# Kernel tuning notes

Measured on AMD Instinct MI355X. Metric: run time of the kernel, lower is better.

Reference implementation:

```python
import jax, jax.numpy as jnp
import numpy as np

N = 50000
E = 800000
IN_C, HID, HEADS, CLS = 128, 64, 5, 40
NEG_SLOPE = 0.2


def gat_conv(h, src, dst, W, a_src, a_dst, bias, heads, out_c, concat):
    n = h.shape[0]
    hp = (h @ W).reshape(n, heads, out_c)            # [N,H,C]
    a_s = jnp.sum(hp * a_src, axis=-1)               # [N,H]
    a_d = jnp.sum(hp * a_dst, axis=-1)               # [N,H]
    e = jax.nn.leaky_relu(a_s[src] + a_d[dst], NEG_SLOPE)  # [Etot,H]
    m = jax.ops.segment_max(e, dst, num_segments=n)  # segment softmax over dst
    e = jnp.exp(e - m[dst])
    s = jax.ops.segment_sum(e, dst, num_segments=n)
    alpha = e / (s[dst] + 1e-16)                     # [Etot,H]
    msg = hp[src] * alpha[:, :, None]                # [Etot,H,C]
    out = jax.ops.segment_sum(msg, dst, num_segments=n)
    if concat:
        out = out.reshape(n, heads * out_c)
    else:
        out = out.mean(axis=1)
    return out + bias


def setup_inputs() -> dict:
    key = jax.random.key(0)
    ks = jax.random.split(key, 12)
    x = jax.random.normal(ks[0], (N, IN_C), dtype=jnp.float32)
    edge_index = jax.random.randint(ks[1], (2, E), 0, N, dtype=jnp.int64)
    g = 0.1
    return {
        "x": x,
        "edge_index": edge_index,
        "emb_W": jax.random.normal(ks[2], (IN_C, HID), jnp.float32) * g,
        "emb_b": jnp.zeros((HID,), jnp.float32),
        "W1": jax.random.normal(ks[3], (HID, HEADS * HID), jnp.float32) * g,
        "att_src1": jax.random.normal(ks[4], (HEADS, HID), jnp.float32) * g,
        "att_dst1": jax.random.normal(ks[5], (HEADS, HID), jnp.float32) * g,
        "b1": jnp.zeros((HEADS * HID,), jnp.float32),
        "W2": jax.random.normal(ks[6], (HEADS * HID, HEADS * CLS), jnp.float32) * g,
        "att_src2": jax.random.normal(ks[7], (HEADS, CLS), jnp.float32) * g,
        "att_dst2": jax.random.normal(ks[8], (HEADS, CLS), jnp.float32) * g,
        "b2": jnp.zeros((CLS,), jnp.float32),
    }


def reference(x, edge_index, emb_W, emb_b, W1, att_src1, att_dst1, b1,
              W2, att_src2, att_dst2, b2):
    n = x.shape[0]
    loops = jnp.arange(n, dtype=edge_index.dtype)
    src = jnp.concatenate([edge_index[0], loops])  # PyG adds self-loops
    dst = jnp.concatenate([edge_index[1], loops])
    h = x @ emb_W + emb_b
    emb = h
    # dropout skipped (eval mode)
    h = jax.nn.elu(gat_conv(h, src, dst, W1, att_src1, att_dst1, b1, HEADS, HID, True))
    h = gat_conv(h, src, dst, W2, att_src2, att_dst2, b2, HEADS, CLS, False)
    return emb, jax.nn.log_softmax(h, axis=1)
```

## Files before the change

kernel.cpp:

```cpp
#include <hip/hip_runtime.h>
#include <math.h>

constexpr int N_NODES = 50000;
constexpr int E_EDGES = 800000;
constexpr int ETOT    = E_EDGES + N_NODES;
constexpr int IN_C    = 128;
constexpr int HID     = 64;
constexpr int HEADS   = 5;
constexpr int CLS     = 40;
constexpr int SLOTW   = 96;
constexpr float NEG_SLOPE = 0.2f;

typedef __attribute__((ext_vector_type(8))) short short8;
typedef __attribute__((ext_vector_type(4))) float float4v;
typedef __attribute__((ext_vector_type(2))) float f32x2;

__device__ __forceinline__ float lrelu(float v) {
    return v > 0.f ? v : NEG_SLOPE * v;
}
__device__ __forceinline__ float bf2f(unsigned short u) {
    return __uint_as_float(((unsigned)u) << 16);
}
__device__ __forceinline__ f32x2 bfp2f(unsigned u) {
    f32x2 r;
    r.x = __uint_as_float(u << 16);
    r.y = __uint_as_float(u & 0xFFFF0000u);
    return r;
}
__device__ __forceinline__ unsigned short f2bf(float f) {
    unsigned u = __float_as_uint(f);
    return (unsigned short)((u + 0x7fffu + ((u >> 16) & 1u)) >> 16);
}

__device__ __forceinline__ void pack_one(const float* __restrict__ B,
                                         unsigned short* __restrict__ Bp,
                                         int N, int KS, int t)
{
    int lane = t & 63;
    int f = (t >> 6) & 3;
    int rest = t >> 8;
    int ks = rest % KS;
    int nt = rest / KS;
    int n = nt * 64 + f * 16 + (lane & 15);
    int kbase = ks * 32 + (lane >> 4) * 8;
    unsigned short vals[8];
    #pragma unroll
    for (int j = 0; j < 8; j++) {
        float v = (n < N) ? B[(long)(kbase + j) * N + n] : 0.f;
        vals[j] = f2bf(v);
    }
    *(ushort4*)(Bp + (long)t * 8)     = make_ushort4(vals[0], vals[1], vals[2], vals[3]);
    *(ushort4*)(Bp + (long)t * 8 + 4) = make_ushort4(vals[4], vals[5], vals[6], vals[7]);
}

__global__ void pack_weights(const float* __restrict__ W0, const float* __restrict__ W1,
                             const float* __restrict__ W2,
                             const float* __restrict__ att1s, const float* __restrict__ att1d,
                             const float* __restrict__ att2s, const float* __restrict__ att2d,
                             unsigned short* __restrict__ Bp0,
                             unsigned short* __restrict__ Bp1,
                             unsigned short* __restrict__ Bp2,
                             float* __restrict__ u1s, float* __restrict__ u1d,
                             unsigned short* __restrict__ Bs)
{
    int t = blockIdx.x * blockDim.x + threadIdx.x;
    if (t < 13824) {
        if (t < 1024)      pack_one(W0, Bp0, 64,  4,  t);
        else if (t < 3584) pack_one(W1, Bp1, 320, 2,  t - 1024);
        else               pack_one(W2, Bp2, 200, 10, t - 3584);
    } else if (t < 14464) {
        int i = t - 13824;
        bool isd = i >= 320;
        int j = isd ? i - 320 : i;
        int h = j >> 6, k = j & 63;
        const float* att = isd ? att1d : att1s;
        float sum = 0.f;
        for (int c = 0; c < 64; c++)
            sum += W1[k * 320 + h * 64 + c] * att[h * 64 + c];
        (isd ? u1d : u1s)[j] = sum;
    } else if (t < 15104) {
        int i = t - 14464;
        int lane = i & 63, ks = i >> 6;
        int n = lane & 15, kq = lane >> 4;
        unsigned short vals[8];
        #pragma unroll
        for (int j = 0; j < 8; j++) {
            int k = ks * 32 + kq * 8 + j;
            float sum = 0.f;
            if (n < 5) {
                for (int c = 0; c < 40; c++)
                    sum += W2[k * 200 + n * 40 + c] * att2s[n * 40 + c];
            } else if (n >= 8 && n < 13) {
                int h = n - 8;
                for (int c = 0; c < 40; c++)
                    sum += W2[k * 200 + h * 40 + c] * att2d[h * 40 + c];
            }
            vals[j] = f2bf(sum);
        }
        *(ushort4*)(Bs + (long)i * 8)     = make_ushort4(vals[0], vals[1], vals[2], vals[3]);
        *(ushort4*)(Bs + (long)i * 8 + 4) = make_ushort4(vals[4], vals[5], vals[6], vals[7]);
    }
}

__global__ __launch_bounds__(256) void emb_scatter_fused(
    const float* __restrict__ A, const unsigned short* __restrict__ Bp,
    const float* __restrict__ bias,
    const float* __restrict__ u1s, const float* __restrict__ u1d,
    float* __restrict__ Cf, unsigned short* __restrict__ Cb,
    float* __restrict__ asd, int M,
    const int* __restrict__ ei, int* __restrict__ cnt,
    unsigned short* __restrict__ slots, int nScat)
{
    if ((int)blockIdx.x < nScat) {
        int t = blockIdx.x * 256 + threadIdx.x;
        if (t >= ETOT) return;
        int s, d;
        if (t < E_EDGES) { s = ei[t]; d = ei[E_EDGES + t]; }
        else             { s = d = t - E_EDGES; }
        int pos = atomicAdd(&cnt[d], 1);
        if (pos < SLOTW) slots[d * SLOTW + pos] = (unsigned short)s;
        return;
    }
    const int gb = blockIdx.x - nScat;
    const int K = 128, KS = 4;
    const int w = threadIdx.x >> 6, lane = threadIdx.x & 63;
    const int cl = lane & 15, kq = lane >> 4;
    int rowA = gb * 64 + w * 16 + cl;
    if (rowA >= M) rowA = M - 1;
    const float* ap = A + (long)rowA * K + kq * 8;
    const unsigned short* bp = Bp + lane * 8;
    float4v acc[4] = {};
    #pragma unroll
    for (int ks = 0; ks < KS; ks++) {
        float4 u0 = *(const float4*)(ap + ks * 32);
        float4 u1 = *(const float4*)(ap + ks * 32 + 4);
        short8 a;
        a[0] = f2bf(u0.x); a[1] = f2bf(u0.y); a[2] = f2bf(u0.z); a[3] = f2bf(u0.w);
        a[4] = f2bf(u1.x); a[5] = f2bf(u1.y); a[6] = f2bf(u1.z); a[7] = f2bf(u1.w);
        #pragma unroll
        for (int f = 0; f < 4; f++) {
            short8 b = *(const short8*)(bp + ks * 2048 + f * 512);
            acc[f] = __builtin_amdgcn_mfma_f32_16x16x32_bf16(a, b, acc[f], 0, 0, 0);
        }
    }
    int rbase = gb * 64 + w * 16 + kq * 4;
    float bc4[4];
    #pragma unroll
    for (int f = 0; f < 4; f++) {
        int col = f * 16 + cl;
        float bc = bias[col];
        bc4[f] = bc;
        #pragma unroll
        for (int r = 0; r < 4; r++) {
            int row = rbase + r;
            if (row < M) {
                float v = acc[f][r] + bc;
                Cf[(long)row * 64 + col] = v;
                Cb[(long)row * 64 + col] = f2bf(v);
            }
        }
    }
    #pragma unroll
    for (int h = 0; h < HEADS; h++) {
        float us[4], ud[4];
        #pragma unroll
        for (int f = 0; f < 4; f++) {
            us[f] = u1s[h * 64 + f * 16 + cl];
            ud[f] = u1d[h * 64 + f * 16 + cl];
        }
        #pragma unroll
        for (int r = 0; r < 4; r++) {
            float ps = 0.f, pd = 0.f;
            #pragma unroll
            for (int f = 0; f < 4; f++) {
                float v = acc[f][r] + bc4[f];
                ps += v * us[f];
                pd += v * ud[f];
            }
            #pragma unroll
            for (int off = 1; off < 16; off <<= 1) {
                ps += __shfl_xor(ps, off);
                pd += __shfl_xor(pd, off);
            }
            int row = rbase + r;
            if (cl == 0 && row < M) {
                asd[row * 16 + h]     = ps;
                asd[row * 16 + 8 + h] = pd;
            }
        }
    }
}

__global__ __launch_bounds__(256) void aggr1_new(
    const int* __restrict__ cnt, const unsigned short* __restrict__ slots,
    const float* __restrict__ asd,
    const unsigned short* __restrict__ emb, unsigned short* __restrict__ e_out)
{
    __shared__ float alph[4][64 * 8];
    int wid = (blockIdx.x * blockDim.x + threadIdx.x) >> 6;
    int w = threadIdx.x >> 6;
    int lane = threadIdx.x & 63;
    if (wid >= N_NODES) return;
    int deg = cnt[wid];
    if (deg > SLOTW) deg = SLOTW;
    const unsigned short* myslot = slots + wid * SLOTW;

    float adh[HEADS];
    #pragma unroll
    for (int h = 0; h < HEADS; h++) adh[h] = asd[wid * 16 + 8 + h];

    const char* embB = (const char*)emb;

    if (deg <= 64) {
        bool has = lane < deg;
        int s = has ? (int)myslot[lane] : 0;
        int rowoff = s * 128;
        float4 s4 = *(const float4*)(asd + s * 16);
        float  s5 = asd[s * 16 + 4];
        float v[HEADS], mx[HEADS], sm[HEADS];
        v[0] = has ? lrelu(s4.x + adh[0]) : -1e30f;
        v[1] = has ? lrelu(s4.y + adh[1]) : -1e30f;
        v[2] = has ? lrelu(s4.z + adh[2]) : -1e30f;
        v[3] = has ? lrelu(s4.w + adh[3]) : -1e30f;
        v[4] = has ? lrelu(s5   + adh[4]) : -1e30f;
        #pragma unroll
        for (int h = 0; h < HEADS; h++) mx[h] = v[h];
        if (deg <= 32) {
            #pragma unroll
            for (int h = 0; h < HEADS; h++)
                #pragma unroll
                for (int off = 16; off; off >>= 1)
                    mx[h] = fmaxf(mx[h], __shfl_xor(mx[h], off));
        } else {
            #pragma unroll
            for (int h = 0; h < HEADS; h++)
                #pragma unroll
                for (int off = 32; off; off >>= 1)
                    mx[h] = fmaxf(mx[h], __shfl_xor(mx[h], off));
        }
        #pragma unroll
        for (int h = 0; h < HEADS; h++) {
            float e = has ? __expf(v[h] - mx[h]) : 0.f;
            v[h] = e;
            sm[h] = e;
        }
        if (deg <= 32) {
            #pragma unroll
            for (int h = 0; h < HEADS; h++)
                #pragma unroll
                for (int off = 16; off; off >>= 1)
                    sm[h] += __shfl_xor(sm[h], off);
        } else {
            #pragma unroll
            for (int h = 0; h < HEADS; h++)
                #pragma unroll
                for (int off = 32; off; off >>= 1)
                    sm[h] += __shfl_xor(sm[h], off);
        }
        #pragma unroll
        for (int h = 0; h < HEADS; h++)
            alph[w][lane * 8 + h] = v[h] / (sm[h] + 1e-16f);

        const int g = lane >> 4, cl16 = lane & 15;
        f32x2 av[HEADS][2] = {};
        int nE8 = (deg + 7) & ~7;
        for (int i = 0; i < nE8; i += 8) {
            int e0 = i + g, e1 = i + 4 + g;
            int off0 = __shfl(rowoff, e0);
            int off1 = __shfl(rowoff, e1);
            uint2 q0 = *(const uint2*)(embB + off0 + cl16 * 8);
            uint2 q1 = *(const uint2*)(embB + off1 + cl16 * 8);
            float4 b0 = *(const float4*)&alph[w][e0 * 8];
            float  b4 = alph[w][e0 * 8 + 4];
            float4 c0 = *(const float4*)&alph[w][e1 * 8];
            float  c4 = alph[w][e1 * 8 + 4];
            f32x2 f0a = bfp2f(q0.x), f0b = bfp2f(q0.y);
            f32x2 f1a = bfp2f(q1.x), f1b = bfp2f(q1.y);
            av[0][0] += f0a * b0.x; av[0][1] += f0b * b0.x;
            av[1][0] += f0a * b0.y; av[1][1] += f0b * b0.y;
            av[2][0] += f0a * b0.z; av[2][1] += f0b * b0.z;
            av[3][0] += f0a * b0.w; av[3][1] += f0b * b0.w;
            av[4][0] += f0a * b4;   av[4][1] += f0b * b4;
            av[0][0] += f1a * c0.x; av[0][1] += f1b * c0.x;
            av[1][0] += f1a * c0.y; av[1][1] += f1b * c0.y;
            av[2][0] += f1a * c0.z; av[2][1] += f1b * c0.z;
            av[3][0] += f1a * c0.w; av[3][1] += f1b * c0.w;
            av[4][0] += f1a * c4;   av[4][1] += f1b * c4;
        }
        #pragma unroll
        for (int h = 0; h < HEADS; h++)
            #pragma unroll
            for (int p = 0; p < 2; p++) {
                float tx = av[h][p].x, ty = av[h][p].y;
                tx += __shfl_xor(tx, 16); tx += __shfl_xor(tx, 32);
                ty += __shfl_xor(ty, 16); ty += __shfl_xor(ty, 32);
                av[h][p].x = tx; av[h][p].y = ty;
            }
        if (g == 0) {
            #pragma unroll
            for (int h = 0; h < HEADS; h++) {
                ushort4 o = make_ushort4(f2bf(av[h][0].x), f2bf(av[h][0].y),
                                         f2bf(av[h][1].x), f2bf(av[h][1].y));
                *(ushort4*)(e_out + (long)wid * 320 + h * 64 + cl16 * 4) = o;
            }
        }
    } else {
        float acc[HEADS] = {};
        float mx[HEADS], inv[HEADS], sm[HEADS] = {};
        #pragma unroll
        for (int h = 0; h < HEADS; h++) mx[h] = -1e30f;
        for (int e = lane; e < deg; e += 64) {
            int s = myslot[e];
            #pragma unroll
            for (int h = 0; h < HEADS; h++)
                mx[h] = fmaxf(mx[h], lrelu(asd[s * 16 + h] + adh[h]));
        }
        #pragma unroll
        for (int h = 0; h < HEADS; h++)
            #pragma unroll
            for (int off = 32; off; off >>= 1)
                mx[h] = fmaxf(mx[h], __shfl_xor(mx[h], off));
        for (int e = lane; e < deg; e += 64) {
            int s = myslot[e];
            #pragma unroll
            for (int h = 0; h < HEADS; h++)
                sm[h] += __expf(lrelu(asd[s * 16 + h] + adh[h]) - mx[h]);
        }
        #pragma unroll
        for (int h = 0; h < HEADS; h++) {
            #pragma unroll
            for (int off = 32; off; off >>= 1)
                sm[h] += __shfl_xor(sm[h], off);
            inv[h] = 1.f / (sm[h] + 1e-16f);
        }
        for (int e = 0; e < deg; e++) {
            int s0 = myslot[e];
            float fv = bf2f(*(const unsigned short*)(embB + s0 * 128 + lane * 2));
            #pragma unroll
            for (int h = 0; h < HEADS; h++) {
                float a0 = __expf(lrelu(asd[s0 * 16 + h] + adh[h]) - mx[h]) * inv[h];
                acc[h] += fv * a0;
            }
        }
        #pragma unroll
        for (int h = 0; h < HEADS; h++)
            e_out[(long)wid * 320 + h * 64 + lane] = f2bf(acc[h]);
    }
}

__global__ __launch_bounds__(256, 5) void gemm_mix_l2(
    const unsigned short* __restrict__ A, const unsigned short* __restrict__ Bp1,
    const unsigned short* __restrict__ Bp2, const float* __restrict__ bias,
    const unsigned short* __restrict__ Bs,
    unsigned short* __restrict__ hp2, float* __restrict__ asd, int M)
{
    constexpr int LDP = 328;
    __shared__ unsigned short tile[32 * LDP];
    const int wid = threadIdx.x >> 6, lane = threadIdx.x & 63;
    const int band = wid >> 1, half = wid & 1;
    const int cl = lane & 15, kq = lane >> 4;
    int rowA = blockIdx.x * 32 + band * 16 + cl;
    if (rowA >= M) rowA = M - 1;
    const unsigned short* ap = A + (long)rowA * 320;
    const unsigned short* bp1 = Bp1 + lane * 8;

    const int rbase = blockIdx.x * 32 + band * 16 + kq * 4;
    const int lrow = band * 16 + kq * 4;

    if (half == 0) {
        float4v acc[12] = {};
        #pragma unroll
        for (int i = 0; i < 3; i++)
            #pragma unroll
            for (int ks = 0; ks < 2; ks++) {
                short8 a = *(const short8*)(ap + i * 64 + ks * 32 + kq * 8);
                #pragma unroll
                for (int f = 0; f < 4; f++) {
                    short8 b = *(const short8*)(bp1 + (i * 2 + ks) * 2048 + f * 512);
                    acc[i * 4 + f] =
                        __builtin_amdgcn_mfma_f32_16x16x32_bf16(a, b, acc[i * 4 + f], 0, 0, 0);
                }
            }
        #pragma unroll
        for (int i = 0; i < 3; i++)
            #pragma unroll
            for (int f = 0; f < 4; f++) {
                int col = i * 64 + f * 16 + cl;
                float bc = bias[col];
                #pragma unroll
                for (int r = 0; r < 4; r++) {
                    float v = acc[i * 4 + f][r] + bc;
                    v = v > 0.f ? v : __expf(v) - 1.f;
                    tile[(lrow + r) * LDP + col] = f2bf(v);
                }
            }
    } else {
        float4v acc[8] = {};
        #pragma unroll
        for (int i = 0; i < 2; i++)
            #pragma unroll
            for (int ks = 0; ks < 2; ks++) {
                short8 a = *(const short8*)(ap + (3 + i) * 64 + ks * 32 + kq * 8);
                #pragma unroll
                for (int f = 0; f < 4; f++) {
                    short8 b = *(const short8*)(bp1 + ((3 + i) * 2 + ks) * 2048 + f * 512);
                    acc[i * 4 + f] =
                        __builtin_amdgcn_mfma_f32_16x16x32_bf16(a, b, acc[i * 4 + f], 0, 0, 0);
                }
            }
        #pragma unroll
        for (int i = 0; i < 2; i++)
            #pragma unroll
            for (int f = 0; f < 4; f++) {
                int col = (3 + i) * 64 + f * 16 + cl;
                float bc = bias[col];
                #pragma unroll
                for (int r = 0; r < 4; r++) {
                    float v = acc[i * 4 + f][r] + bc;
                    v = v > 0.f ? v : __expf(v) - 1.f;
                    tile[(lrow + r) * LDP + col] = f2bf(v);
                }
            }
    }
    __syncthreads();

    const unsigned short* arow = tile + (band * 16 + cl) * LDP;
    const unsigned short* bp2 = Bp2 + lane * 8;
    const unsigned short* bs  = Bs + lane * 8;
    float4v acc2[8] = {};
    float4v accs = {};
    #pragma unroll
    for (int ks = 0; ks < 10; ks++) {
        short8 a2 = *(const short8*)(arow + ks * 32 + kq * 8);
        if (half == 0) {
            short8 b = *(const short8*)(bs + ks * 512);
            accs = __builtin_amdgcn_mfma_f32_16x16x32_bf16(a2, b, accs, 0, 0, 0);
        }
        #pragma unroll
        for (int nt2 = 0; nt2 < 2; nt2++)
            #pragma unroll
            for (int f = 0; f < 4; f++) {
                short8 b = *(const short8*)(bp2 + (((half * 2 + nt2) * 10 + ks) * 2048) + f * 512);
                acc2[nt2 * 4 + f] =
                    __builtin_amdgcn_mfma_f32_16x16x32_bf16(a2, b, acc2[nt2 * 4 + f], 0, 0, 0);
            }
    }
    if (half == 0) {
        #pragma unroll
        for (int r = 0; r < 4; r++) {
            int row = rbase + r;
            if (row < M) asd[row * 16 + cl] = accs[r];
        }
    }
    #pragma unroll
    for (int nt2 = 0; nt2 < 2; nt2++)
        #pragma unroll
        for (int f = 0; f < 4; f++) {
            int col = (half * 2 + nt2) * 64 + f * 16 + cl;
            if (col >= 200) continue;
            #pragma unroll
            for (int r = 0; r < 4; r++) {
                int row = rbase + r;
                if (row < M) hp2[(long)row * 200 + col] = f2bf(acc2[nt2 * 4 + f][r]);
            }
        }
}

__global__ __launch_bounds__(256) void aggr2_fused(
    const int* __restrict__ cnt, const unsigned short* __restrict__ slots,
    const float* __restrict__ asd,
    const unsigned short* __restrict__ hp, const float* __restrict__ bias,
    float* __restrict__ out)
{
    __shared__ float alph[4][320];
    int wid = (blockIdx.x * blockDim.x + threadIdx.x) >> 6;
    int w = threadIdx.x >> 6;
    int lane = threadIdx.x & 63;
    if (wid >= N_NODES) return;
    int deg = cnt[wid];
    if (deg > SLOTW) deg = SLOTW;
    const unsigned short* myslot = slots + wid * SLOTW;

    float adh[HEADS];
    #pragma unroll
    for (int h = 0; h < HEADS; h++) adh[h] = asd[wid * 16 + 8 + h];

    const bool act = lane < 50;
    const int ch4 = lane * 4;
    const int hq  = act ? lane / 10 : 0;
    const char* hpB = (const char*)hp;
    f32x2 acc01 = {0.f, 0.f}, acc23 = {0.f, 0.f};

    if (deg <= 64) {
        bool has = lane < deg;
        int s = has ? (int)myslot[lane] : 0;
        int rowoff = s * 400;
        float4 s4 = *(const float4*)(asd + s * 16);
        float  s5 = asd[s * 16 + 4];
        float v[HEADS], mx[HEADS], sm[HEADS];
        v[0] = has ? lrelu(s4.x + adh[0]) : -1e30f;
        v[1] = has ? lrelu(s4.y + adh[1]) : -1e30f;
        v[2] = has ? lrelu(s4.z + adh[2]) : -1e30f;
        v[3] = has ? lrelu(s4.w + adh[3]) : -1e30f;
        v[4] = has ? lrelu(s5   + adh[4]) : -1e30f;
        #pragma unroll
        for (int h = 0; h < HEADS; h++) mx[h] = v[h];
        if (deg <= 32) {
            #pragma unroll
            for (int h = 0; h < HEADS; h++)
                #pragma unroll
                for (int off = 16; off; off >>= 1)
                    mx[h] = fmaxf(mx[h], __shfl_xor(mx[h], off));
        } else {
            #pragma unroll
            for (int h = 0; h < HEADS; h++)
                #pragma unroll
                for (int off = 32; off; off >>= 1)
                    mx[h] = fmaxf(mx[h], __shfl_xor(mx[h], off));
        }
        #pragma unroll
        for (int h = 0; h < HEADS; h++) {
            float e = has ? __expf(v[h] - mx[h]) : 0.f;
            v[h] = e;
            sm[h] = e;
        }
        if (deg <= 32) {
            #pragma unroll
            for (int h = 0; h < HEADS; h++)
                #pragma unroll
                for (int off = 16; off; off >>= 1)
                    sm[h] += __shfl_xor(sm[h], off);
        } else {
            #pragma unroll
            for (int h = 0; h < HEADS; h++)
                #pragma unroll
                for (int off = 32; off; off >>= 1)
                    sm[h] += __shfl_xor(sm[h], off);
        }
        if (has) {
            #pragma unroll
            for (int h = 0; h < HEADS; h++)
                alph[w][lane * 5 + h] = 0.2f * v[h] / (sm[h] + 1e-16f);
        }
        int i = 0;
        for (; i + 7 < deg; i += 8) {
            uint2 q[8]; float a[8];
            #pragma unroll
            for (int k = 0; k < 8; k++) {
                int off = __shfl(rowoff, i + k);
                q[k] = act ? *(const uint2*)(hpB + off + ch4 * 2)
                           : make_uint2(0u, 0u);
                a[k] = alph[w][(i + k) * 5 + hq];
            }
            #pragma unroll
            for (int k = 0; k < 8; k++) {
                f32x2 fa = bfp2f(q[k].x), fb = bfp2f(q[k].y);
                acc01 += fa * a[k];
                acc23 += fb * a[k];
            }
        }
        for (; i < deg; i++) {
            int off = __shfl(rowoff, i);
            if (act) {
                uint2 q0 = *(const uint2*)(hpB + off + ch4 * 2);
                float a0 = alph[w][i * 5 + hq];
                f32x2 fa = bfp2f(q0.x), fb = bfp2f(q0.y);
                acc01 += fa * a0;
                acc23 += fb * a0;
            }
        }
    } else {
        float mx[HEADS], inv[HEADS], sm[HEADS] = {};
        #pragma unroll
        for (int h = 0; h < HEADS; h++) mx[h] = -1e30f;
        for (int e = lane; e < deg; e += 64) {
            int s = myslot[e];
            #pragma unroll
            for (int h = 0; h < HEADS; h++)
                mx[h] = fmaxf(mx[h], lrelu(asd[s * 16 + h] + adh[h]));
        }
        #pragma unroll
        for (int h = 0; h < HEADS; h++)
            #pragma unroll
            for (int off = 32; off; off >>= 1)
                mx[h] = fmaxf(mx[h], __shfl_xor(mx[h], off));
        for (int e = lane; e < deg; e += 64) {
            int s = myslot[e];
            #pragma unroll
            for (int h = 0; h < HEADS; h++)
                sm[h] += __expf(lrelu(asd[s * 16 + h] + adh[h]) - mx[h]);
        }
        #pragma unroll
        for (int h = 0; h < HEADS; h++) {
            #pragma unroll
            for (int off = 32; off; off >>= 1)
                sm[h] += __shfl_xor(sm[h], off);
            inv[h] = 0.2f / (sm[h] + 1e-16f);
        }
        for (int e = 0; e < deg; e++) {
            int s0 = myslot[e];
            if (act) {
                uint2 q0 = *(const uint2*)(hpB + s0 * 400 + ch4 * 2);
                float a0 = __expf(lrelu(asd[s0 * 16 + hq] + adh[hq]) - mx[hq]) * inv[hq];
                f32x2 fa = bfp2f(q0.x), fb = bfp2f(q0.y);
                acc01 += fa * a0;
                acc23 += fb * a0;
            }
        }
    }

    float acc0 = acc01.x, acc1 = acc01.y, acc2 = acc23.x, acc3 = acc23.y;
    float r0 = acc0, r1 = acc1, r2 = acc2, r3 = acc3;
    #pragma unroll
    for (int h5 = 1; h5 < 5; h5++) {
        int sl = (lane + 10 * h5) & 63;
        r0 += __shfl(acc0, sl);
        r1 += __shfl(acc1, sl);
        r2 += __shfl(acc2, sl);
        r3 += __shfl(acc3, sl);
    }

    float vb0 = -1e30f, vb1 = -1e30f, vb2 = -1e30f, vb3 = -1e30f;
    if (lane < 10) {
        vb0 = r0 + bias[ch4 + 0];
        vb1 = r1 + bias[ch4 + 1];
        vb2 = r2 + bias[ch4 + 2];
        vb3 = r3 + bias[ch4 + 3];
    }
    float mxv = fmaxf(fmaxf(vb0, vb1), fmaxf(vb2, vb3));
    #pragma unroll
    for (int off = 32; off; off >>= 1)
        mxv = fmaxf(mxv, __shfl_xor(mxv, off));
    float sme = 0.f;
    if (lane < 10)
        sme = __expf(vb0 - mxv) + __expf(vb1 - mxv) +
              __expf(vb2 - mxv) + __expf(vb3 - mxv);
    #pragma unroll
    for (int off = 32; off; off >>= 1)
        sme += __shfl_xor(sme, off);
    float ls = mxv + __logf(sme);
    if (lane < 10) {
        float4 o = make_float4(vb0 - ls, vb1 - ls, vb2 - ls, vb3 - ls);
        *(float4*)(out + (long)wid * CLS + ch4) = o;
    }
}

extern "C" void kernel_launch(void* const* d_in, const int* in_sizes, int n_in,
                              void* d_out, int out_size, void* d_ws, size_t ws_size,
                              hipStream_t stream)
{
    const float* x     = (const float*)d_in[0];
    const int*   ei    = (const int*)d_in[1];
    const float* emb_W = (const float*)d_in[2];
    const float* emb_b = (const float*)d_in[3];
    const float* W1    = (const float*)d_in[4];
    const float* as1   = (const float*)d_in[5];
    const float* ad1   = (const float*)d_in[6];
    const float* b1    = (const float*)d_in[7];
    const float* W2    = (const float*)d_in[8];
    const float* as2   = (const float*)d_in[9];
    const float* ad2   = (const float*)d_in[10];
    const float* b2    = (const float*)d_in[11];

    float* out_emb = (float*)d_out;
    float* out_cls = (float*)d_out + (size_t)N_NODES * HID;

    char* ws = (char*)d_ws;
    unsigned short* e_agg  = (unsigned short*)(ws);
    unsigned short* hp2b   = (unsigned short*)(ws + 32000000);
    float*          asd1   = (float*)(ws + 52000000);
    float*          asd2   = (float*)(ws + 55200000);
    unsigned short* embb   = (unsigned short*)(ws + 64000000);
    unsigned short* Bp0    = (unsigned short*)(ws + 74400000);
    unsigned short* Bp1    = (unsigned short*)(ws + 74500000);
    unsigned short* Bp2    = (unsigned short*)(ws + 74600000);
    float*          u1s    = (float*)(ws + 74800000);
    float*          u1d    = (float*)(ws + 74810000);
    unsigned short* Bs     = (unsigned short*)(ws + 74820000);
    int*            cnt    = (int*)(ws + 74840000);
    unsigned short* slots  = (unsigned short*)(ws + 75100000);

    const dim3 blk(256);
    const int nb4  = (N_NODES + 3) / 4;
    const int mgrid  = (N_NODES + 63) / 64;
    const int mgrid2 = (N_NODES + 31) / 32;
    const int nScat  = (ETOT + 255) / 256;
    const int pgrid  = (15104 + 255) / 256;

    hipMemsetAsync(cnt, 0, (size_t)N_NODES * 4, stream);
    pack_weights<<<pgrid, blk, 0, stream>>>(emb_W, W1, W2, as1, ad1, as2, ad2,
                                            Bp0, Bp1, Bp2, u1s, u1d, Bs);

    emb_scatter_fused<<<nScat + mgrid, blk, 0, stream>>>(
        x, Bp0, emb_b, u1s, u1d, out_emb, embb, asd1, N_NODES,
        ei, cnt, slots, nScat);

    aggr1_new<<<nb4, blk, 0, stream>>>(cnt, slots, asd1, embb, e_agg);

    gemm_mix_l2<<<mgrid2, blk, 0, stream>>>(e_agg, Bp1, Bp2, b1, Bs,
                                            hp2b, asd2, N_NODES);

    aggr2_fused<<<nb4, blk, 0, stream>>>(cnt, slots, asd2, hp2b, b2, out_cls);
}
```

Baseline: 350.1 us.

## Pad degree counters, pre-seed self-loops, batch edge scatter atomics per thread

Degree counters now sit at a 16-int stride so atomics on different destinations fall in separate cache lines. The pack kernel seeds each node's count to 1 and writes its self-loop into slot 0, which removes the memset launch and the self-loop scatter work. The scatter now has each thread load four edges and issue four atomics, putting several memory operations in flight per thread. The padded counters take 16x more memory (about 3.2MB), and the self-loop now always holds slot 0, changing which edges are dropped when a node's degree exceeds the slot width.

```diff
diff --git a/kernel.cpp b/kernel.cpp
--- a/kernel.cpp
+++ b/kernel.cpp
@@ -9,6 +9,7 @@
 constexpr int HEADS   = 5;
 constexpr int CLS     = 40;
 constexpr int SLOTW   = 96;
+constexpr int CSTR    = 16;
 constexpr float NEG_SLOPE = 0.2f;
 
 typedef __attribute__((ext_vector_type(8))) short short8;
@@ -61,7 +62,8 @@
                              unsigned short* __restrict__ Bp1,
                              unsigned short* __restrict__ Bp2,
                              float* __restrict__ u1s, float* __restrict__ u1d,
-                             unsigned short* __restrict__ Bs)
+                             unsigned short* __restrict__ Bs,
+                             int* __restrict__ cnt, unsigned short* __restrict__ slots)
 {
     int t = blockIdx.x * blockDim.x + threadIdx.x;
     if (t < 13824) {
@@ -100,6 +102,10 @@
         *(ushort4*)(Bs + (long)i * 8)     = make_ushort4(vals[0], vals[1], vals[2], vals[3]);
         *(ushort4*)(Bs + (long)i * 8 + 4) = make_ushort4(vals[4], vals[5], vals[6], vals[7]);
     }
+    if (t < N_NODES) {
+        cnt[t * CSTR] = 1;
+        slots[t * SLOTW] = (unsigned short)t;
+    }
 }
 
 __global__ __launch_bounds__(256) void emb_scatter_fused(
@@ -112,13 +118,24 @@
     unsigned short* __restrict__ slots, int nScat)
 {
     if ((int)blockIdx.x < nScat) {
-        int t = blockIdx.x * 256 + threadIdx.x;
-        if (t >= ETOT) return;
-        int s, d;
-        if (t < E_EDGES) { s = ei[t]; d = ei[E_EDGES + t]; }
-        else             { s = d = t - E_EDGES; }
-        int pos = atomicAdd(&cnt[d], 1);
-        if (pos < SLOTW) slots[d * SLOTW + pos] = (unsigned short)s;
+        int base = blockIdx.x * 1024 + threadIdx.x;
+        int s[4], d[4], pos[4];
+        bool ok[4];
+        #pragma unroll
+        for (int j = 0; j < 4; j++) {
+            int t = base + j * 256;
+            ok[j] = t < E_EDGES;
+            int tt = ok[j] ? t : 0;
+            s[j] = ei[tt];
+            d[j] = ei[E_EDGES + tt];
+        }
+        #pragma unroll
+        for (int j = 0; j < 4; j++)
+            pos[j] = ok[j] ? atomicAdd(&cnt[d[j] * CSTR], 1) : SLOTW;
+        #pragma unroll
+        for (int j = 0; j < 4; j++)
+            if (pos[j] < SLOTW)
+                slots[d[j] * SLOTW + pos[j]] = (unsigned short)s[j];
         return;
     }
     const int gb = blockIdx.x - nScat;
@@ -201,7 +218,7 @@
     int w = threadIdx.x >> 6;
     int lane = threadIdx.x & 63;
     if (wid >= N_NODES) return;
-    int deg = cnt[wid];
+    int deg = cnt[wid * CSTR];
     if (deg > SLOTW) deg = SLOTW;
     const unsigned short* myslot = slots + wid * SLOTW;
 
@@ -477,7 +494,7 @@
     int w = threadIdx.x >> 6;
     int lane = threadIdx.x & 63;
     if (wid >= N_NODES) return;
-    int deg = cnt[wid];
+    int deg = cnt[wid * CSTR];
     if (deg > SLOTW) deg = SLOTW;
     const unsigned short* myslot = slots + wid * SLOTW;
 
@@ -670,6 +687,7 @@
     unsigned short* hp2b   = (unsigned short*)(ws + 32000000);
     float*          asd1   = (float*)(ws + 52000000);
     float*          asd2   = (float*)(ws + 55200000);
+    int*            cnt    = (int*)(ws + 58400000);
     unsigned short* embb   = (unsigned short*)(ws + 64000000);
     unsigned short* Bp0    = (unsigned short*)(ws + 74400000);
     unsigned short* Bp1    = (unsigned short*)(ws + 74500000);
@@ -677,19 +695,18 @@
     float*          u1s    = (float*)(ws + 74800000);
     float*          u1d    = (float*)(ws + 74810000);
     unsigned short* Bs     = (unsigned short*)(ws + 74820000);
-    int*            cnt    = (int*)(ws + 74840000);
     unsigned short* slots  = (unsigned short*)(ws + 75100000);
 
     const dim3 blk(256);
     const int nb4  = (N_NODES + 3) / 4;
     const int mgrid  = (N_NODES + 63) / 64;
     const int mgrid2 = (N_NODES + 31) / 32;
-    const int nScat  = (ETOT + 255) / 256;
-    const int pgrid  = (15104 + 255) / 256;
-
-    hipMemsetAsync(cnt, 0, (size_t)N_NODES * 4, stream);
+    const int nScat  = (E_EDGES + 1023) / 1024;
+    const int pgrid  = (N_NODES + 255) / 256;
+
     pack_weights<<<pgrid, blk, 0, stream>>>(emb_W, W1, W2, as1, ad1, as2, ad2,
-                                            Bp0, Bp1, Bp2, u1s, u1d, Bs);
+                                            Bp0, Bp1, Bp2, u1s, u1d, Bs,
+                                            cnt, slots);
 
     emb_scatter_fused<<<nScat + mgrid, blk, 0, stream>>>(
         x, Bp0, emb_b, u1s, u1d, out_emb, embb, asd1, N_NODES,
```

New measurement: 328.4 us. 1.07x faster.
